# Kernel optimization log

Hardware: AMD Instinct MI355X
Metric: run time of the kernel (lower is better)

Reference implementation:

```python
import jax, jax.numpy as jnp
import numpy as np

DMODEL = 1024
H = 16
DK = DMODEL // H


def setup_inputs() -> dict:
    key = jax.random.key(0)
    ks = jax.random.split(key, 11)
    B, S = 4, 2048
    scale = 1.0 / np.sqrt(DMODEL)
    inp = {
        'Q': jax.random.normal(ks[0], (B, S, DMODEL), jnp.float32),
        'K': jax.random.normal(ks[1], (B, S, DMODEL), jnp.float32),
        'V': jax.random.normal(ks[2], (B, S, DMODEL), jnp.float32),
        'wq_w': jax.random.normal(ks[3], (DMODEL, DMODEL), jnp.float32) * scale,
        'wq_b': jnp.zeros((DMODEL,), jnp.float32),
        'wk_w': jax.random.normal(ks[4], (DMODEL, DMODEL), jnp.float32) * scale,
        'wk_b': jnp.zeros((DMODEL,), jnp.float32),
        'wv_w': jax.random.normal(ks[5], (DMODEL, DMODEL), jnp.float32) * scale,
        'wv_b': jnp.zeros((DMODEL,), jnp.float32),
        'out_w': jax.random.normal(ks[6], (DMODEL, DMODEL), jnp.float32) * scale,
        'out_b': jnp.zeros((DMODEL,), jnp.float32),
    }
    return inp


def _split_heads(x, B):
    # [B, S, dmodel] -> [B, H, S, DK]
    return x.reshape(B, -1, H, DK).transpose(0, 2, 1, 3)


def reference(Q, K, V, wq_w, wq_b, wk_w, wk_b, wv_w, wv_b, out_w, out_b):
    B, S, _ = Q.shape
    q = _split_heads(Q @ wq_w.T + wq_b, B)  # [B,H,S,DK]
    k = _split_heads(K @ wk_w.T + wk_b, B)
    v = _split_heads(V @ wv_w.T + wv_b, B)
    energy = jnp.einsum('bhqd,bhkd->bhqk', q, k) / jnp.sqrt(jnp.asarray(DK, q.dtype))
    attn = jax.nn.softmax(energy, axis=-1)
    context = jnp.einsum('bhqk,bhkd->bhqd', attn, v)  # [B,H,S,DK]
    context = context.transpose(0, 2, 1, 3).reshape(B, S, DMODEL)
    return context @ out_w.T + out_b
```

## Files before the change

### kernel.cpp

```cpp
#include <hip/hip_runtime.h>
#include <hip/hip_bf16.h>
#include <stdint.h>

#define DMODEL 1024
#define SEQ    2048
#define BATCH  4
#define NH     16
#define DKH    64
#define MROWS  (BATCH*SEQ)

typedef unsigned short u16;
typedef __bf16 bf8 __attribute__((ext_vector_type(8)));
typedef float  f4  __attribute__((ext_vector_type(4)));
typedef float  fv4 __attribute__((ext_vector_type(4)));
typedef unsigned int u32x4 __attribute__((ext_vector_type(4)));
typedef unsigned int u32x2 __attribute__((ext_vector_type(2)));

__device__ __forceinline__ u16 f2b(float f) {
  __bf16 h = (__bf16)f;
  return __builtin_bit_cast(u16, h);
}

__device__ __forceinline__ float exp2_fast(float x) {
#if __has_builtin(__builtin_amdgcn_exp2f)
  return __builtin_amdgcn_exp2f(x);
#else
  return exp2f(x);
#endif
}

__device__ __forceinline__ void plswap32(unsigned& a, unsigned& b) {
#if __has_builtin(__builtin_amdgcn_permlane32_swap)
  u32x2 r = __builtin_amdgcn_permlane32_swap(a, b, false, false);
  a = r[0]; b = r[1];
#else
  asm("v_permlane32_swap_b32 %0, %1" : "+v"(a), "+v"(b));
#endif
}
__device__ __forceinline__ void plswap16(unsigned& a, unsigned& b) {
#if __has_builtin(__builtin_amdgcn_permlane16_swap)
  u32x2 r = __builtin_amdgcn_permlane16_swap(a, b, false, false);
  a = r[0]; b = r[1];
#else
  asm("v_permlane16_swap_b32 %0, %1" : "+v"(a), "+v"(b));
#endif
}

#define GLL16(gp, lp) __builtin_amdgcn_global_load_lds( \
    (const __attribute__((address_space(1))) void*)(gp), \
    (__attribute__((address_space(3))) void*)(lp), 16, 0, 0)

#define MFMA16(a, b, c) __builtin_amdgcn_mfma_f32_16x16x32_bf16((a), (b), (c), 0, 0, 0)

struct CvtArgs {
  const float* src[7];
  u16* dst[7];
  int n8[7];
};

__global__ __launch_bounds__(256) void cvt_all(CvtArgs a) {
  const int r = blockIdx.y;
  const float* __restrict__ s = a.src[r];
  u16* __restrict__ d = a.dst[r];
  const int n8 = a.n8[r];
  for (int i = blockIdx.x * 256 + threadIdx.x; i < n8; i += gridDim.x * 256) {
    fv4 x = *(const fv4*)(s + (size_t)i * 8);
    fv4 y = *(const fv4*)(s + (size_t)i * 8 + 4);
    u32x4 o;
    o[0] = (unsigned)f2b(x[0]) | ((unsigned)f2b(x[1]) << 16);
    o[1] = (unsigned)f2b(x[2]) | ((unsigned)f2b(x[3]) << 16);
    o[2] = (unsigned)f2b(y[0]) | ((unsigned)f2b(y[1]) << 16);
    o[3] = (unsigned)f2b(y[2]) | ((unsigned)f2b(y[3]) << 16);
    *(u32x4*)(d + (size_t)i * 8) = o;
  }
}

template<int MODE>
__device__ __forceinline__ void gemm_core(const u16* __restrict__ A,
                                          const u16* __restrict__ Bw,
                                          const float* __restrict__ bias,
                                          void* __restrict__ Cout,
                                          int bx, int by) {
  __shared__ u16 As[128 * 32];
  __shared__ u16 Bs[128 * 32];
  const int tid = threadIdx.x;
  const int w = tid >> 6, l = tid & 63, g = l >> 4, ln = l & 15;
  const int m0 = by * 128, n0 = bx * 128;
  const int wm = (w >> 1) * 64, wn = (w & 1) * 64;
  const f4 zero = {0.f, 0.f, 0.f, 0.f};
  f4 acc[4][4];
#pragma unroll
  for (int i = 0; i < 4; ++i)
#pragma unroll
    for (int j = 0; j < 4; ++j) acc[i][j] = zero;

  for (int ks = 0; ks < DMODEL / 32; ++ks) {
    __syncthreads();
#pragma unroll
    for (int p = 0; p < 2; ++p) {
      int j = p * 256 + tid;
      int row = j >> 2, cs = j & 3;
      int sc = cs ^ ((row >> 1) & 3);
      GLL16(A + (size_t)(m0 + row) * DMODEL + ks * 32 + sc * 8,
            &As[(p * 256 + w * 64) * 8]);
      GLL16(Bw + (size_t)(n0 + row) * DMODEL + ks * 32 + sc * 8,
            &Bs[(p * 256 + w * 64) * 8]);
    }
    __syncthreads();

    bf8 af[4], bfr[4];
#pragma unroll
    for (int mt = 0; mt < 4; ++mt) {
      int row = wm + mt * 16 + ln;
      af[mt] = *(const bf8*)((const char*)As + row * 64 + ((g ^ ((row >> 1) & 3)) << 4));
    }
#pragma unroll
    for (int nt = 0; nt < 4; ++nt) {
      int row = wn + nt * 16 + ln;
      bfr[nt] = *(const bf8*)((const char*)Bs + row * 64 + ((g ^ ((row >> 1) & 3)) << 4));
    }
#pragma unroll
    for (int mt = 0; mt < 4; ++mt)
#pragma unroll
      for (int nt = 0; nt < 4; ++nt)
        acc[mt][nt] = MFMA16(af[mt], bfr[nt], acc[mt][nt]);
  }

#pragma unroll
  for (int nt = 0; nt < 4; ++nt) {
    int col = n0 + wn + nt * 16 + ln;
    float bv = bias[col];
#pragma unroll
    for (int mt = 0; mt < 4; ++mt) {
      int mrow = m0 + wm + mt * 16 + g * 4;
#pragma unroll
      for (int r = 0; r < 4; ++r) {
        float v = acc[mt][nt][r] + bv;
        int m = mrow + r;
        if (MODE == 2) {
          ((float*)Cout)[(size_t)m * DMODEL + col] = v;
        } else if (MODE == 0) {
          ((u16*)Cout)[(size_t)m * DMODEL + col] = f2b(v);
        } else if (MODE == 3) {
          ((u16*)Cout)[(size_t)m * DMODEL + col] = f2b(v * 0.18033688f);
        } else {
          int b = m >> 11, s2 = m & 2047;
          ((u16*)Cout)[((size_t)(b * 1024 + col)) * SEQ + s2] = f2b(v);
        }
      }
    }
  }
}

__global__ __launch_bounds__(256) void gemm_qkv(
    const u16* __restrict__ Qb, const u16* __restrict__ Kb, const u16* __restrict__ Vb,
    const u16* __restrict__ Wq, const u16* __restrict__ Wk, const u16* __restrict__ Wv,
    const float* __restrict__ bq, const float* __restrict__ bk, const float* __restrict__ bv,
    u16* __restrict__ Qp, u16* __restrict__ Kp, u16* __restrict__ Vpt) {
  if (blockIdx.z == 0)      gemm_core<3>(Qb, Wq, bq, Qp,  blockIdx.x, blockIdx.y);
  else if (blockIdx.z == 1) gemm_core<0>(Kb, Wk, bk, Kp,  blockIdx.x, blockIdx.y);
  else                      gemm_core<1>(Vb, Wv, bv, Vpt, blockIdx.x, blockIdx.y);
}

__global__ __launch_bounds__(256) void gemm_out(
    const u16* __restrict__ Ctx, const u16* __restrict__ Wo,
    const float* __restrict__ bo, float* __restrict__ Out) {
  gemm_core<2>(Ctx, Wo, bo, Out, blockIdx.x, blockIdx.y);
}

__global__ __launch_bounds__(256) void attn_kernel(
    const u16* __restrict__ Qp, const u16* __restrict__ Kp,
    const u16* __restrict__ Vpt, u16* __restrict__ Ctx) {
  __shared__ u16 Klds[2][64 * 64];
  __shared__ u16 Vlds[2][64 * 64];
  const int tid = threadIdx.x, w = tid >> 6, l = tid & 63, g = l >> 4, ln = l & 15;
  const int qc = blockIdx.x, bh = blockIdx.y, h = bh & 15;
  const size_t qkrow = (size_t)(bh >> 4) * SEQ;
  const size_t vrow = (size_t)bh * DKH;
  const int q0 = qc * 64 + w * 16;

  bf8 qf[2];
#pragma unroll
  for (int c = 0; c < 2; ++c)
    qf[c] = *(const bf8*)(Qp + (qkrow + q0 + ln) * DMODEL + h * DKH + c * 32 + g * 8);

  auto stage = [&](int t, int buf) {
#pragma unroll
    for (int p = 0; p < 2; ++p) {
      int j = p * 256 + tid;
      int row = j >> 3, cs = j & 7;
      int sc = cs ^ (row & 7);
      GLL16(Kp + (qkrow + t * 64 + row) * DMODEL + h * DKH + sc * 8,
            &Klds[buf][(p * 256 + w * 64) * 8]);
      GLL16(Vpt + (vrow + row) * SEQ + t * 64 + sc * 8,
            &Vlds[buf][(p * 256 + w * 64) * 8]);
    }
  };

  const f4 zero = {0.f, 0.f, 0.f, 0.f};
  f4 o[4];
#pragma unroll
  for (int dt = 0; dt < 4; ++dt) o[dt] = zero;
  float l_run = 0.f;

  stage(0, 0);
  __syncthreads();

  for (int t = 0; t < SEQ / 64; ++t) {
    const int cur = t & 1;
    if (t < SEQ / 64 - 1) stage(t + 1, cur ^ 1);

    f4 sf[4];
    __builtin_amdgcn_s_setprio(1);
#pragma unroll
    for (int kt = 0; kt < 4; ++kt) {
      f4 s = zero;
#pragma unroll
      for (int c = 0; c < 2; ++c) {
        int row = kt * 16 + ln;
        bf8 kf = *(const bf8*)((const char*)Klds[cur] + row * 128 +
                               ((((c << 2) | g) ^ (row & 7)) << 4));
        s = MFMA16(kf, qf[c], s);
      }
      sf[kt] = s;
    }
    __builtin_amdgcn_s_setprio(0);

    float pv[16];
#pragma unroll
    for (int kt = 0; kt < 4; ++kt)
#pragma unroll
      for (int r = 0; r < 4; ++r) pv[kt * 4 + r] = exp2_fast(sf[kt][r]);
    float psum[4];
#pragma unroll
    for (int kt = 0; kt < 4; ++kt)
      psum[kt] = (pv[kt * 4] + pv[kt * 4 + 1]) + (pv[kt * 4 + 2] + pv[kt * 4 + 3]);
    float sum = (psum[0] + psum[1]) + (psum[2] + psum[3]);
    sum += __shfl_xor(sum, 16);
    sum += __shfl_xor(sum, 32);
    l_run += sum;

    unsigned pp[4][2];
#pragma unroll
    for (int kt = 0; kt < 4; ++kt)
#pragma unroll
      for (int r2 = 0; r2 < 2; ++r2)
        pp[kt][r2] = (unsigned)f2b(pv[kt * 4 + 2 * r2]) |
                     ((unsigned)f2b(pv[kt * 4 + 2 * r2 + 1]) << 16);

    union { u32x4 u; bf8 f; } pa[2];
#pragma unroll
    for (int c = 0; c < 2; ++c)
#pragma unroll
      for (int r2 = 0; r2 < 2; ++r2) {
        unsigned Areg = pp[2 * c][r2], Breg = pp[2 * c + 1][r2];
        plswap32(Areg, Breg);
        plswap16(Areg, Breg);
        pa[c].u[r2] = Areg;
        pa[c].u[2 + r2] = Breg;
      }

#pragma unroll
    for (int c = 0; c < 2; ++c) {
      __builtin_amdgcn_s_setprio(1);
#pragma unroll
      for (int dt = 0; dt < 4; ++dt) {
        int row = dt * 16 + ln;
        bf8 vf = *(const bf8*)((const char*)Vlds[cur] + row * 128 +
                               ((((c << 2) | g) ^ (row & 7)) << 4));
        o[dt] = MFMA16(pa[c].f, vf, o[dt]);
      }
      __builtin_amdgcn_s_setprio(0);
    }

    __syncthreads();
  }

  float inv[4];
#pragma unroll
  for (int r = 0; r < 4; ++r) inv[r] = 1.0f / __shfl(l_run, g * 4 + r);
#pragma unroll
  for (int dt = 0; dt < 4; ++dt)
#pragma unroll
    for (int r = 0; r < 4; ++r)
      Ctx[(qkrow + q0 + g * 4 + r) * DMODEL + h * DKH + dt * 16 + ln] =
          f2b(o[dt][r] * inv[r]);
}

extern "C" void kernel_launch(void* const* d_in, const int* in_sizes, int n_in,
                              void* d_out, int out_size, void* d_ws, size_t ws_size,
                              hipStream_t stream) {
  const float* Q    = (const float*)d_in[0];
  const float* K    = (const float*)d_in[1];
  const float* V    = (const float*)d_in[2];
  const float* wq_w = (const float*)d_in[3];
  const float* wq_b = (const float*)d_in[4];
  const float* wk_w = (const float*)d_in[5];
  const float* wk_b = (const float*)d_in[6];
  const float* wv_w = (const float*)d_in[7];
  const float* wv_b = (const float*)d_in[8];
  const float* ow_w = (const float*)d_in[9];
  const float* ow_b = (const float*)d_in[10];

  char* ws = (char*)d_ws;
  const size_t SZ = (size_t)MROWS * DMODEL * 2;
  const size_t WZ = (size_t)DMODEL * DMODEL * 2;
  u16* Qb  = (u16*)(ws);
  u16* Kb  = (u16*)(ws + SZ);
  u16* Vb  = (u16*)(ws + 2 * SZ);
  u16* Wqb = (u16*)(ws + 3 * SZ);
  u16* Wkb = (u16*)(ws + 3 * SZ + WZ);
  u16* Wvb = (u16*)(ws + 3 * SZ + 2 * WZ);
  u16* Wob = (u16*)(ws + 3 * SZ + 3 * WZ);
  u16* Qp  = (u16*)(ws + 3 * SZ + 4 * WZ);
  u16* Kp  = (u16*)(ws + 4 * SZ + 4 * WZ);
  u16* Vpt = (u16*)(ws + 5 * SZ + 4 * WZ);
  u16* Ctx = (u16*)(ws + 6 * SZ + 4 * WZ);

  CvtArgs ca;
  ca.src[0] = Q;    ca.dst[0] = Qb;  ca.n8[0] = MROWS * DMODEL / 8;
  ca.src[1] = K;    ca.dst[1] = Kb;  ca.n8[1] = MROWS * DMODEL / 8;
  ca.src[2] = V;    ca.dst[2] = Vb;  ca.n8[2] = MROWS * DMODEL / 8;
  ca.src[3] = wq_w; ca.dst[3] = Wqb; ca.n8[3] = DMODEL * DMODEL / 8;
  ca.src[4] = wk_w; ca.dst[4] = Wkb; ca.n8[4] = DMODEL * DMODEL / 8;
  ca.src[5] = wv_w; ca.dst[5] = Wvb; ca.n8[5] = DMODEL * DMODEL / 8;
  ca.src[6] = ow_w; ca.dst[6] = Wob; ca.n8[6] = DMODEL * DMODEL / 8;

  dim3 blk(256);
  cvt_all<<<dim3(512, 7), blk, 0, stream>>>(ca);

  dim3 gq(DMODEL / 128, MROWS / 128, 3);
  gemm_qkv<<<gq, blk, 0, stream>>>(Qb, Kb, Vb, Wqb, Wkb, Wvb,
                                   wq_b, wk_b, wv_b, Qp, Kp, Vpt);

  dim3 ga(SEQ / 64, BATCH * NH);
  attn_kernel<<<ga, blk, 0, stream>>>(Qp, Kp, Vpt, Ctx);

  dim3 go(DMODEL / 128, MROWS / 128);
  gemm_out<<<go, blk, 0, stream>>>(Ctx, Wob, ow_b, (float*)d_out);
}
```

Measured before the change: 385.9 us.

## Split V projection into LDS-transposed GEMM, swizzle block order, MFMA row sums

The V projection moves into its own GEMM kernel. It stages the output tile through LDS and writes the transposed V with coalesced 16-byte stores, replacing the old scattered 2-byte transposed stores. All GEMM and attention launches now use 1D grids with an XCD-style block swizzle so neighbouring tiles share L2 on the same die. The attention kernel drops the shuffle-based softmax row sum and accumulates the denominator with an extra MFMA against a vector of ones. That costs one more MFMA per chunk and sums bf16-rounded probabilities rather than fp32 ones.

```diff
diff --git a/kernel.cpp b/kernel.cpp
--- a/kernel.cpp
+++ b/kernel.cpp
@@ -141,31 +141,116 @@
           ((float*)Cout)[(size_t)m * DMODEL + col] = v;
         } else if (MODE == 0) {
           ((u16*)Cout)[(size_t)m * DMODEL + col] = f2b(v);
-        } else if (MODE == 3) {
+        } else {
           ((u16*)Cout)[(size_t)m * DMODEL + col] = f2b(v * 0.18033688f);
-        } else {
-          int b = m >> 11, s2 = m & 2047;
-          ((u16*)Cout)[((size_t)(b * 1024 + col)) * SEQ + s2] = f2b(v);
         }
       }
     }
   }
 }
 
-__global__ __launch_bounds__(256) void gemm_qkv(
-    const u16* __restrict__ Qb, const u16* __restrict__ Kb, const u16* __restrict__ Vb,
-    const u16* __restrict__ Wq, const u16* __restrict__ Wk, const u16* __restrict__ Wv,
-    const float* __restrict__ bq, const float* __restrict__ bk, const float* __restrict__ bv,
-    u16* __restrict__ Qp, u16* __restrict__ Kp, u16* __restrict__ Vpt) {
-  if (blockIdx.z == 0)      gemm_core<3>(Qb, Wq, bq, Qp,  blockIdx.x, blockIdx.y);
-  else if (blockIdx.z == 1) gemm_core<0>(Kb, Wk, bk, Kp,  blockIdx.x, blockIdx.y);
-  else                      gemm_core<1>(Vb, Wv, bv, Vpt, blockIdx.x, blockIdx.y);
+__global__ __launch_bounds__(256) void gemm_qk(
+    const u16* __restrict__ Qb, const u16* __restrict__ Kb,
+    const u16* __restrict__ Wq, const u16* __restrict__ Wk,
+    const float* __restrict__ bq, const float* __restrict__ bk,
+    u16* __restrict__ Qp, u16* __restrict__ Kp) {
+  const int bid = blockIdx.x;
+  const int swz = (bid & 7) * 128 + (bid >> 3);
+  const int z = swz >> 9, rem = swz & 511;
+  const int by = rem >> 3, bx = rem & 7;
+  if (z == 0) gemm_core<3>(Qb, Wq, bq, Qp, bx, by);
+  else        gemm_core<0>(Kb, Wk, bk, Kp, bx, by);
 }
 
 __global__ __launch_bounds__(256) void gemm_out(
     const u16* __restrict__ Ctx, const u16* __restrict__ Wo,
     const float* __restrict__ bo, float* __restrict__ Out) {
-  gemm_core<2>(Ctx, Wo, bo, Out, blockIdx.x, blockIdx.y);
+  const int bid = blockIdx.x;
+  const int swz = (bid & 7) * 64 + (bid >> 3);
+  gemm_core<2>(Ctx, Wo, bo, Out, swz & 7, swz >> 3);
+}
+
+__global__ __launch_bounds__(256) void gemm_v(
+    const u16* __restrict__ A, const u16* __restrict__ Bw,
+    const float* __restrict__ bias, u16* __restrict__ Vt) {
+  alignas(16) __shared__ u16 sm[128 * 136];
+  u16* As = sm;
+  u16* Bs = sm + 4096;
+  const int bid = blockIdx.x;
+  const int swz = (bid & 7) * 64 + (bid >> 3);
+  const int by = swz >> 3, bx = swz & 7;
+  const int tid = threadIdx.x;
+  const int w = tid >> 6, l = tid & 63, g = l >> 4, ln = l & 15;
+  const int m0 = by * 128, n0 = bx * 128;
+  const int wm = (w >> 1) * 64, wn = (w & 1) * 64;
+  const f4 zero = {0.f, 0.f, 0.f, 0.f};
+  f4 acc[4][4];
+#pragma unroll
+  for (int i = 0; i < 4; ++i)
+#pragma unroll
+    for (int j = 0; j < 4; ++j) acc[i][j] = zero;
+
+  for (int ks = 0; ks < DMODEL / 32; ++ks) {
+    __syncthreads();
+#pragma unroll
+    for (int p = 0; p < 2; ++p) {
+      int j = p * 256 + tid;
+      int row = j >> 2, cs = j & 3;
+      int sc = cs ^ ((row >> 1) & 3);
+      GLL16(A + (size_t)(m0 + row) * DMODEL + ks * 32 + sc * 8,
+            &As[(p * 256 + w * 64) * 8]);
+      GLL16(Bw + (size_t)(n0 + row) * DMODEL + ks * 32 + sc * 8,
+            &Bs[(p * 256 + w * 64) * 8]);
+    }
+    __syncthreads();
+
+    bf8 af[4], bfr[4];
+#pragma unroll
+    for (int mt = 0; mt < 4; ++mt) {
+      int row = wm + mt * 16 + ln;
+      af[mt] = *(const bf8*)((const char*)As + row * 64 + ((g ^ ((row >> 1) & 3)) << 4));
+    }
+#pragma unroll
+    for (int nt = 0; nt < 4; ++nt) {
+      int row = wn + nt * 16 + ln;
+      bfr[nt] = *(const bf8*)((const char*)Bs + row * 64 + ((g ^ ((row >> 1) & 3)) << 4));
+    }
+#pragma unroll
+    for (int mt = 0; mt < 4; ++mt)
+#pragma unroll
+      for (int nt = 0; nt < 4; ++nt)
+        acc[mt][nt] = MFMA16(af[mt], bfr[nt], acc[mt][nt]);
+  }
+
+  __syncthreads();
+
+#pragma unroll
+  for (int nt = 0; nt < 4; ++nt) {
+    int n_loc = wn + nt * 16 + ln;
+    float bv = bias[n0 + n_loc];
+#pragma unroll
+    for (int mt = 0; mt < 4; ++mt) {
+      int m_base = wm + mt * 16 + g * 4;
+      u32x2 pk;
+      pk[0] = (unsigned)f2b(acc[mt][nt][0] + bv) |
+              ((unsigned)f2b(acc[mt][nt][1] + bv) << 16);
+      pk[1] = (unsigned)f2b(acc[mt][nt][2] + bv) |
+              ((unsigned)f2b(acc[mt][nt][3] + bv) << 16);
+      *(u32x2*)&sm[n_loc * 136 + m_base] = pk;
+    }
+  }
+  __syncthreads();
+
+  const int b = m0 >> 11;
+  const size_t vbase = (size_t)(b * 1024 + n0);
+  const int s0 = m0 & 2047;
+#pragma unroll
+  for (int it = 0; it < 8; ++it) {
+    int task = it * 256 + tid;
+    int n = task >> 4, e = task & 15;
+    u32x4 v = *(const u32x4*)&sm[n * 136 + e * 8];
+    *(u32x4*)&Vt[(vbase + n) * SEQ + s0 + e * 8] = v;
+  }
 }
 
 __global__ __launch_bounds__(256) void attn_kernel(
@@ -174,7 +259,9 @@
   __shared__ u16 Klds[2][64 * 64];
   __shared__ u16 Vlds[2][64 * 64];
   const int tid = threadIdx.x, w = tid >> 6, l = tid & 63, g = l >> 4, ln = l & 15;
-  const int qc = blockIdx.x, bh = blockIdx.y, h = bh & 15;
+  const int bid = blockIdx.x;
+  const int swz = (bid & 7) * 256 + (bid >> 3);
+  const int qc = swz & 31, bh = swz >> 5, h = bh & 15;
   const size_t qkrow = (size_t)(bh >> 4) * SEQ;
   const size_t vrow = (size_t)bh * DKH;
   const int q0 = qc * 64 + w * 16;
@@ -183,6 +270,10 @@
 #pragma unroll
   for (int c = 0; c < 2; ++c)
     qf[c] = *(const bf8*)(Qp + (qkrow + q0 + ln) * DMODEL + h * DKH + c * 32 + g * 8);
+
+  union { u16 s[8]; bf8 f; } ones;
+#pragma unroll
+  for (int i = 0; i < 8; ++i) ones.s[i] = 0x3F80;
 
   auto stage = [&](int t, int buf) {
 #pragma unroll
@@ -201,7 +292,7 @@
   f4 o[4];
 #pragma unroll
   for (int dt = 0; dt < 4; ++dt) o[dt] = zero;
-  float l_run = 0.f;
+  f4 lacc = zero;
 
   stage(0, 0);
   __syncthreads();
@@ -226,27 +317,16 @@
     }
     __builtin_amdgcn_s_setprio(0);
 
-    float pv[16];
-#pragma unroll
-    for (int kt = 0; kt < 4; ++kt)
-#pragma unroll
-      for (int r = 0; r < 4; ++r) pv[kt * 4 + r] = exp2_fast(sf[kt][r]);
-    float psum[4];
-#pragma unroll
-    for (int kt = 0; kt < 4; ++kt)
-      psum[kt] = (pv[kt * 4] + pv[kt * 4 + 1]) + (pv[kt * 4 + 2] + pv[kt * 4 + 3]);
-    float sum = (psum[0] + psum[1]) + (psum[2] + psum[3]);
-    sum += __shfl_xor(sum, 16);
-    sum += __shfl_xor(sum, 32);
-    l_run += sum;
-
     unsigned pp[4][2];
 #pragma unroll
-    for (int kt = 0; kt < 4; ++kt)
-#pragma unroll
-      for (int r2 = 0; r2 < 2; ++r2)
-        pp[kt][r2] = (unsigned)f2b(pv[kt * 4 + 2 * r2]) |
-                     ((unsigned)f2b(pv[kt * 4 + 2 * r2 + 1]) << 16);
+    for (int kt = 0; kt < 4; ++kt) {
+      float p0 = exp2_fast(sf[kt][0]);
+      float p1 = exp2_fast(sf[kt][1]);
+      float p2 = exp2_fast(sf[kt][2]);
+      float p3 = exp2_fast(sf[kt][3]);
+      pp[kt][0] = (unsigned)f2b(p0) | ((unsigned)f2b(p1) << 16);
+      pp[kt][1] = (unsigned)f2b(p2) | ((unsigned)f2b(p3) << 16);
+    }
 
     union { u32x4 u; bf8 f; } pa[2];
 #pragma unroll
@@ -270,6 +350,7 @@
                                ((((c << 2) | g) ^ (row & 7)) << 4));
         o[dt] = MFMA16(pa[c].f, vf, o[dt]);
       }
+      lacc = MFMA16(pa[c].f, ones.f, lacc);
       __builtin_amdgcn_s_setprio(0);
     }
 
@@ -278,7 +359,7 @@
 
   float inv[4];
 #pragma unroll
-  for (int r = 0; r < 4; ++r) inv[r] = 1.0f / __shfl(l_run, g * 4 + r);
+  for (int r = 0; r < 4; ++r) inv[r] = 1.0f / lacc[r];
 #pragma unroll
   for (int dt = 0; dt < 4; ++dt)
 #pragma unroll
@@ -329,13 +410,10 @@
   dim3 blk(256);
   cvt_all<<<dim3(512, 7), blk, 0, stream>>>(ca);
 
-  dim3 gq(DMODEL / 128, MROWS / 128, 3);
-  gemm_qkv<<<gq, blk, 0, stream>>>(Qb, Kb, Vb, Wqb, Wkb, Wvb,
-                                   wq_b, wk_b, wv_b, Qp, Kp, Vpt);
-
-  dim3 ga(SEQ / 64, BATCH * NH);
-  attn_kernel<<<ga, blk, 0, stream>>>(Qp, Kp, Vpt, Ctx);
-
-  dim3 go(DMODEL / 128, MROWS / 128);
-  gemm_out<<<go, blk, 0, stream>>>(Ctx, Wob, ow_b, (float*)d_out);
-}
+  gemm_qk<<<1024, blk, 0, stream>>>(Qb, Kb, Wqb, Wkb, wq_b, wk_b, Qp, Kp);
+  gemm_v<<<512, blk, 0, stream>>>(Vb, Wvb, wv_b, Vpt);
+
+  attn_kernel<<<2048, blk, 0, stream>>>(Qp, Kp, Vpt, Ctx);
+
+  gemm_out<<<512, blk, 0, stream>>>(Ctx, Wob, ow_b, (float*)d_out);
+}
```

Measured after the change: 371.1 us. 3.9% less time.
